# Optimization experiments

Hardware: AMD Instinct MI355X
Metric: run time of the kernel (lower is better)

## Reference

```python
import jax, jax.numpy as jnp
import numpy as np

N_NODES = 50000
N_EDGES = 800000
IN_DIM = 128
HID = 32
HEADS = 4
OUT_DIM = 64
NEG_SLOPE = 0.2


def _glorot(key, shape):
    fan = shape[0] + shape[-1] if len(shape) > 1 else shape[-1]
    lim = jnp.sqrt(6.0 / fan)
    return jax.random.uniform(key, shape, jnp.float32, -lim, lim)


def setup_inputs() -> dict:
    key = jax.random.key(0)
    ks = jax.random.split(key, 10)
    x = jax.random.normal(ks[0], (N_NODES, IN_DIM), jnp.float32)
    edge_index = jax.random.randint(ks[1], (2, N_EDGES), 0, N_NODES, jnp.int32)
    # layer 1: in=IN_DIM, heads=HEADS, out=HID, concat
    W1 = _glorot(ks[2], (IN_DIM, HEADS * HID))
    a_src1 = _glorot(ks[3], (HEADS, HID))
    a_dst1 = _glorot(ks[4], (HEADS, HID))
    b1 = jnp.zeros((HEADS * HID,), jnp.float32)
    # layer 2: in=HEADS*HID, heads=1, out=OUT_DIM, mean
    W2 = _glorot(ks[5], (HEADS * HID, OUT_DIM))
    a_src2 = _glorot(ks[6], (1, OUT_DIM))
    a_dst2 = _glorot(ks[7], (1, OUT_DIM))
    b2 = jnp.zeros((OUT_DIM,), jnp.float32)
    return {"x": x, "edge_index": edge_index, "W1": W1, "a_src1": a_src1,
            "a_dst1": a_dst1, "b1": b1, "W2": W2, "a_src2": a_src2,
            "a_dst2": a_dst2, "b2": b2}


def gat_conv(x, src, dst, W, a_src, a_dst, bias, heads, out_ch, concat, num_nodes):
    # x: [N, in]; src/dst: [E] (self-loops already included)
    h = (x @ W).reshape(num_nodes, heads, out_ch)          # [N, H, F]
    alpha_s = jnp.einsum('nhf,hf->nh', h, a_src)           # [N, H]
    alpha_d = jnp.einsum('nhf,hf->nh', h, a_dst)
    e = alpha_s[src] + alpha_d[dst]                        # [E, H]
    e = jnp.where(e >= 0, e, NEG_SLOPE * e)                # leaky relu
    # segment softmax over destination neighborhoods
    e_max = jax.ops.segment_max(e, dst, num_segments=num_nodes)
    ex = jnp.exp(e - e_max[dst])
    denom = jax.ops.segment_sum(ex, dst, num_segments=num_nodes)
    alpha = ex / (denom[dst] + 1e-16)                      # [E, H]
    msg = h[src] * alpha[:, :, None]                       # [E, H, F]
    out = jax.ops.segment_sum(msg, dst, num_segments=num_nodes)  # [N, H, F]
    if concat:
        out = out.reshape(num_nodes, heads * out_ch)
    else:
        out = out.mean(axis=1)
    return out + bias


def reference(x, edge_index, W1, a_src1, a_dst1, b1, W2, a_src2, a_dst2, b2):
    n = x.shape[0]
    # PyG GATConv default add_self_loops=True
    loop = jnp.arange(n, dtype=edge_index.dtype)
    src = jnp.concatenate([edge_index[0], loop])
    dst = jnp.concatenate([edge_index[1], loop])
    h = gat_conv(x, src, dst, W1, a_src1, a_dst1, b1, HEADS, HID, True, n)
    h = jax.nn.relu(h)
    out = gat_conv(h, src, dst, W2, a_src2, a_dst2, b2, 1, OUT_DIM, False, n)
    return out
```

## Files before the change

kernel.cpp:

```cpp
#include <hip/hip_runtime.h>
#include <hip/hip_fp16.h>
#include <math.h>


#define NEG_SLOPE 0.2f
#define CAP 64

__device__ __forceinline__ float lrelu_exp(float e) {
    e = (e >= 0.f) ? e : NEG_SLOPE * e;
    return __expf(e);
}

__global__ __launch_bounds__(256) void build_kernel(
    const float* __restrict__ x, const float* __restrict__ W1,
    const float* __restrict__ a_src1, const float* __restrict__ a_dst1,
    __half* __restrict__ h1h, float* __restrict__ as1, float* __restrict__ ad1,
    const int* __restrict__ src, const int* __restrict__ dst,
    int* __restrict__ deg, unsigned short* __restrict__ col,
    int N, int E, int Gg) {
    __shared__ float Ws[32 * 128];
    __shared__ float xs[64 * 32];
    const int tid = threadIdx.x;

    if (blockIdx.x >= Gg) {
        const int base = (blockIdx.x - Gg) * 2048 + tid * 8;
        int s[8], d[8];
        if (base + 8 <= E) {
            int4 a0 = *(const int4*)&src[base];
            int4 a1 = *(const int4*)&src[base + 4];
            int4 c0 = *(const int4*)&dst[base];
            int4 c1 = *(const int4*)&dst[base + 4];
            s[0]=a0.x; s[1]=a0.y; s[2]=a0.z; s[3]=a0.w;
            s[4]=a1.x; s[5]=a1.y; s[6]=a1.z; s[7]=a1.w;
            d[0]=c0.x; d[1]=c0.y; d[2]=c0.z; d[3]=c0.w;
            d[4]=c1.x; d[5]=c1.y; d[6]=c1.z; d[7]=c1.w;
        } else {
#pragma unroll
            for (int u = 0; u < 8; ++u) {
                int i = base + u;
                if (i < E) { s[u] = src[i]; d[u] = dst[i]; }
                else       { s[u] = -1;     d[u] = -1; }
            }
        }
        int p[8];
#pragma unroll
        for (int u = 0; u < 8; ++u)
            if (d[u] >= 0) p[u] = atomicAdd(&deg[d[u]], 1);
#pragma unroll
        for (int u = 0; u < 8; ++u)
            if (d[u] >= 0 && p[u] < CAP)
                col[d[u] * CAP + p[u]] = (unsigned short)s[u];
        return;
    }

    const int tf = tid & 31;
    const int tn = tid >> 5;
    const int nb = blockIdx.x * 64;
    float acc[8][4];
#pragma unroll
    for (int i = 0; i < 8; ++i)
#pragma unroll
        for (int j = 0; j < 4; ++j) acc[i][j] = 0.f;

    for (int kc = 0; kc < 128; kc += 32) {
#pragma unroll
        for (int l = 0; l < 4; ++l) {
            int idx = tid + l * 256;
            int k = idx >> 5, f4 = idx & 31;
            *(float4*)&Ws[k * 128 + f4 * 4] =
                *(const float4*)&W1[(kc + k) * 128 + f4 * 4];
        }
#pragma unroll
        for (int l = 0; l < 2; ++l) {
            int idx = tid + l * 256;
            int n = idx >> 3, j = idx & 7;
            int gn = nb + n; if (gn >= N) gn = N - 1;
            *(float4*)&xs[n * 32 + j * 4] =
                *(const float4*)&x[gn * 128 + kc + j * 4];
        }
        __syncthreads();
#pragma unroll
        for (int k = 0; k < 32; ++k) {
            float4 w = *(const float4*)&Ws[k * 128 + tf * 4];
#pragma unroll
            for (int i = 0; i < 8; ++i) {
                float xv = xs[(tn * 8 + i) * 32 + k];
                acc[i][0] += xv * w.x; acc[i][1] += xv * w.y;
                acc[i][2] += xv * w.z; acc[i][3] += xv * w.w;
            }
        }
        __syncthreads();
    }
    float4 asv = *(const float4*)&a_src1[tf * 4];
    float4 adv = *(const float4*)&a_dst1[tf * 4];
    const int head = tf >> 3;
    const int lane8 = tf & 7;
#pragma unroll
    for (int i = 0; i < 8; ++i) {
        int n = nb + tn * 8 + i;
        if (n < N) {
            __half2 p0 = __floats2half2_rn(acc[i][0], acc[i][1]);
            __half2 p1 = __floats2half2_rn(acc[i][2], acc[i][3]);
            uint2 pk;
            pk.x = *(unsigned*)&p0;
            pk.y = *(unsigned*)&p1;
            *(uint2*)&h1h[(size_t)n * 128 + tf * 4] = pk;
        }
        float s = acc[i][0]*asv.x + acc[i][1]*asv.y + acc[i][2]*asv.z + acc[i][3]*asv.w;
        float d = acc[i][0]*adv.x + acc[i][1]*adv.y + acc[i][2]*adv.z + acc[i][3]*adv.w;
        s += __shfl_down(s, 4); d += __shfl_down(d, 4);
        s += __shfl_down(s, 2); d += __shfl_down(d, 2);
        s += __shfl_down(s, 1); d += __shfl_down(d, 1);
        if (lane8 == 0 && n < N) { as1[n * 4 + head] = s; ad1[n * 4 + head] = d; }
    }
}

__global__ __launch_bounds__(256, 4) void agg1mm_kernel(
    const __half2* __restrict__ h1h2, const float* __restrict__ as1,
    const float* __restrict__ ad1, const float* __restrict__ b1,
    const float* __restrict__ W2, const float* __restrict__ a_src2,
    const float* __restrict__ a_dst2, const int* __restrict__ deg,
    const unsigned short* __restrict__ col,
    __half* __restrict__ h2h, float* __restrict__ as2, float* __restrict__ ad2,
    int N) {
    __shared__ float wls[4][4][68];
    __shared__ int   cls[4][64];
    __shared__ float hrs[4][128];
    __shared__ float part[16][64];
    const int tid = threadIdx.x;
    const int w = tid >> 6;
    const int lane = tid & 63;
    const int d = blockIdx.x * 4 + w;

    if (d < N) {
        const int hsel = lane >> 4;
        const float4 ad4 = *(const float4*)&ad1[4 * d];
        const float4 asd = *(const float4*)&as1[4 * d];
        const float adh = (hsel == 0) ? ad4.x : (hsel == 1) ? ad4.y
                        : (hsel == 2) ? ad4.z : ad4.w;
        const float ash = (hsel == 0) ? asd.x : (hsel == 1) ? asd.y
                        : (hsel == 2) ? asd.z : asd.w;
        const int dg = min(deg[d], CAP);
        const int dgp = (dg + 31) & ~31;
        const int beg = d * CAP;

        if (lane < dgp) {
            if (lane < dg) {
                int s = (int)col[beg + lane];
                cls[w][lane] = s;
                float4 a4 = *(const float4*)&as1[4 * s];
                wls[w][0][lane] = lrelu_exp(a4.x + ad4.x);
                wls[w][1][lane] = lrelu_exp(a4.y + ad4.y);
                wls[w][2][lane] = lrelu_exp(a4.z + ad4.z);
                wls[w][3][lane] = lrelu_exp(a4.w + ad4.w);
            } else {
                cls[w][lane] = 0;
                wls[w][0][lane] = 0.f;
                wls[w][1][lane] = 0.f;
                wls[w][2][lane] = 0.f;
                wls[w][3][lane] = 0.f;
            }
        }

        float wself = lrelu_exp(ash + adh);
        float2 vself = __half22float2(h1h2[((unsigned)d << 6) | (unsigned)lane]);
        float den = wself, accx = wself * vself.x, accy = wself * vself.y;

        for (int jj = 0; jj < dgp; jj += 32) {
            int ss[32];
#pragma unroll
            for (int q = 0; q < 8; ++q)
                *(int4*)&ss[q * 4] = *(const int4*)&cls[w][jj + q * 4];
            __half2 v[32];
#pragma unroll
            for (int u = 0; u < 32; ++u)
                v[u] = h1h2[(((unsigned)ss[u]) << 6) | (unsigned)lane];
            float wt[32];
#pragma unroll
            for (int q = 0; q < 8; ++q)
                *(float4*)&wt[q * 4] = *(const float4*)&wls[w][hsel][jj + q * 4];
#pragma unroll
            for (int u = 0; u < 32; ++u) {
                float2 vf = __half22float2(v[u]);
                den += wt[u];
                accx = fmaf(wt[u], vf.x, accx);
                accy = fmaf(wt[u], vf.y, accy);
            }
        }
        const float inv = 1.f / (den + 1e-16f);
        float2 bv = *(const float2*)&b1[lane * 2];
        float2 o;
        o.x = fmaxf(fmaf(accx, inv, bv.x), 0.f);
        o.y = fmaxf(fmaf(accy, inv, bv.y), 0.f);
        *(float2*)&hrs[w][lane * 2] = o;
    } else {
        hrs[w][lane * 2] = 0.f;
        hrs[w][lane * 2 + 1] = 0.f;
    }
    __syncthreads();

    float p0 = 0.f, p1 = 0.f, p2 = 0.f, p3 = 0.f;
#pragma unroll
    for (int kk = 0; kk < 32; kk += 4) {
        const int k = w * 32 + kk;
        float4 h0 = *(const float4*)&hrs[0][k];
        float4 h1 = *(const float4*)&hrs[1][k];
        float4 h2 = *(const float4*)&hrs[2][k];
        float4 h3 = *(const float4*)&hrs[3][k];
        float wv0 = W2[(k + 0) * 64 + lane];
        float wv1 = W2[(k + 1) * 64 + lane];
        float wv2 = W2[(k + 2) * 64 + lane];
        float wv3 = W2[(k + 3) * 64 + lane];
        p0 += h0.x * wv0 + h0.y * wv1 + h0.z * wv2 + h0.w * wv3;
        p1 += h1.x * wv0 + h1.y * wv1 + h1.z * wv2 + h1.w * wv3;
        p2 += h2.x * wv0 + h2.y * wv1 + h2.z * wv2 + h2.w * wv3;
        p3 += h3.x * wv0 + h3.y * wv1 + h3.z * wv2 + h3.w * wv3;
    }
    part[w * 4 + 0][lane] = p0;
    part[w * 4 + 1][lane] = p1;
    part[w * 4 + 2][lane] = p2;
    part[w * 4 + 3][lane] = p3;
    __syncthreads();

    if (d < N) {
        float h2f = part[0 * 4 + w][lane] + part[1 * 4 + w][lane] +
                    part[2 * 4 + w][lane] + part[3 * 4 + w][lane];
        h2h[((unsigned)d << 6) | (unsigned)lane] = __float2half(h2f);
        float s = h2f * a_src2[lane];
        float dv = h2f * a_dst2[lane];
        s += __shfl_down(s, 32); dv += __shfl_down(dv, 32);
        s += __shfl_down(s, 16); dv += __shfl_down(dv, 16);
        s += __shfl_down(s, 8);  dv += __shfl_down(dv, 8);
        s += __shfl_down(s, 4);  dv += __shfl_down(dv, 4);
        s += __shfl_down(s, 2);  dv += __shfl_down(dv, 2);
        s += __shfl_down(s, 1);  dv += __shfl_down(dv, 1);
        if (lane == 0) { as2[d] = s; ad2[d] = dv; }
    }
}

__global__ __launch_bounds__(256, 4) void agg2_kernel(
    const __half* __restrict__ h2h, const float* __restrict__ as2,
    const float* __restrict__ ad2, const float* __restrict__ b2,
    const int* __restrict__ deg, const unsigned short* __restrict__ col,
    float* __restrict__ out, int N) {
    __shared__ int   cls[4][64];
    __shared__ float wl[4][64];
    const int lane = threadIdx.x & 63;
    const int w = threadIdx.x >> 6;
    const int d = blockIdx.x * 4 + w;
    if (d >= N) return;
    const int dg = min(deg[d], CAP);
    const int dgp = (dg + 31) & ~31;
    const int beg = d * CAP;
    const float adv = ad2[d];

    float wself = lrelu_exp(as2[d] + adv);
    float den = wself;
    float acc = wself * __half2float(h2h[((unsigned)d << 6) | (unsigned)lane]);

    if (lane < dgp) {
        if (lane < dg) {
            int s = (int)col[beg + lane];
            cls[w][lane] = s;
            wl[w][lane] = lrelu_exp(as2[s] + adv);
        } else {
            cls[w][lane] = 0;
            wl[w][lane] = 0.f;
        }
    }

    for (int jj = 0; jj < dgp; jj += 32) {
        int ss[32];
#pragma unroll
        for (int q = 0; q < 8; ++q)
            *(int4*)&ss[q * 4] = *(const int4*)&cls[w][jj + q * 4];
        __half v[32];
#pragma unroll
        for (int u = 0; u < 32; ++u)
            v[u] = h2h[(((unsigned)ss[u]) << 6) | (unsigned)lane];
        float wt[32];
#pragma unroll
        for (int q = 0; q < 8; ++q)
            *(float4*)&wt[q * 4] = *(const float4*)&wl[w][jj + q * 4];
#pragma unroll
        for (int u = 0; u < 32; ++u) {
            den += wt[u];
            acc = fmaf(wt[u], __half2float(v[u]), acc);
        }
    }
    out[(size_t)d * 64 + lane] = acc / (den + 1e-16f) + b2[lane];
}

extern "C" void kernel_launch(void* const* d_in, const int* in_sizes, int n_in,
                              void* d_out, int out_size, void* d_ws, size_t ws_size,
                              hipStream_t stream) {
    const float* x      = (const float*)d_in[0];
    const int*   eidx   = (const int*)d_in[1];
    const float* W1     = (const float*)d_in[2];
    const float* a_src1 = (const float*)d_in[3];
    const float* a_dst1 = (const float*)d_in[4];
    const float* b1     = (const float*)d_in[5];
    const float* W2     = (const float*)d_in[6];
    const float* a_src2 = (const float*)d_in[7];
    const float* a_dst2 = (const float*)d_in[8];
    const float* b2     = (const float*)d_in[9];
    float* out = (float*)d_out;

    const int N = in_sizes[0] / 128;
    const int E = in_sizes[1] / 2;

    const int* src = eidx;
    const int* dst = eidx + E;

    float* ws_f = (float*)d_ws;
    float* as1 = ws_f;
    float* ad1 = as1 + (size_t)N * 4;
    float* as2 = ad1 + (size_t)N * 4;
    float* ad2 = as2 + (size_t)N;
    __half* h1h = (__half*)(ad2 + (size_t)N);
    __half* h2h = h1h + (size_t)N * 128;
    int* deg = (int*)(h2h + (size_t)N * 64);
    unsigned short* col = (unsigned short*)(deg + N);

    const int Gg = (N + 63) / 64;
    const int Gs = (E + 2047) / 2048;

    hipMemsetAsync(deg, 0, (size_t)N * sizeof(int), stream);

    build_kernel<<<Gg + Gs, 256, 0, stream>>>(x, W1, a_src1, a_dst1,
                                              h1h, as1, ad1,
                                              src, dst, deg, col, N, E, Gg);

    agg1mm_kernel<<<(N + 3) / 4, 256, 0, stream>>>(
        (const __half2*)h1h, as1, ad1, b1, W2, a_src2, a_dst2,
        deg, col, h2h, as2, ad2, N);

    agg2_kernel<<<(N + 3) / 4, 256, 0, stream>>>(h2h, as2, ad2, b2,
                                                 deg, col, out, N);
}
```

Measured before the change: 207.4 us.

## Partition edge scatter by destination range and use fp16 dot2 for layer-2 matmul

```diff
diff --git a/kernel.cpp b/kernel.cpp
--- a/kernel.cpp
+++ b/kernel.cpp
@@ -9,6 +9,16 @@
 __device__ __forceinline__ float lrelu_exp(float e) {
     e = (e >= 0.f) ? e : NEG_SLOPE * e;
     return __expf(e);
+}
+
+typedef _Float16 half2v __attribute__((ext_vector_type(2)));
+__device__ __forceinline__ float fdot2(__half2 a, __half2 b, float c) {
+#if __has_builtin(__builtin_amdgcn_fdot2)
+    return __builtin_amdgcn_fdot2(*(half2v*)&a, *(half2v*)&b, c, false);
+#else
+    float2 af = __half22float2(a), bf = __half22float2(b);
+    return fmaf(af.x, bf.x, fmaf(af.y, bf.y, c));
+#endif
 }
 
 __global__ __launch_bounds__(256) void build_kernel(
@@ -17,13 +27,29 @@
     __half* __restrict__ h1h, float* __restrict__ as1, float* __restrict__ ad1,
     const int* __restrict__ src, const int* __restrict__ dst,
     int* __restrict__ deg, unsigned short* __restrict__ col,
-    int N, int E, int Gg) {
+    const float* __restrict__ W2, __half2* __restrict__ W2p,
+    int N, int E, int Gg, int Gs8) {
     __shared__ float Ws[32 * 128];
     __shared__ float xs[64 * 32];
     const int tid = threadIdx.x;
 
+    if (blockIdx.x >= Gg + Gs8) {
+#pragma unroll
+        for (int it = 0; it < 16; ++it) {
+            int idx = it * 256 + tid;
+            int kp = idx >> 6, n = idx & 63;
+            W2p[idx] = __floats2half2_rn(W2[(2 * kp) * 64 + n],
+                                         (W2[(2 * kp + 1) * 64 + n]));
+        }
+        return;
+    }
+
     if (blockIdx.x >= Gg) {
-        const int base = (blockIdx.x - Gg) * 2048 + tid * 8;
+        const int part = blockIdx.x & 7;
+        const int stripe = (blockIdx.x - Gg) >> 3;
+        const int psz = (N + 7) / 8;
+        const int dlo = part * psz;
+        const int base = stripe * 2048 + tid * 8;
         int s[8], d[8];
         if (base + 8 <= E) {
             int4 a0 = *(const int4*)&src[base];
@@ -39,17 +65,16 @@
             for (int u = 0; u < 8; ++u) {
                 int i = base + u;
                 if (i < E) { s[u] = src[i]; d[u] = dst[i]; }
-                else       { s[u] = -1;     d[u] = -1; }
-            }
-        }
-        int p[8];
-#pragma unroll
-        for (int u = 0; u < 8; ++u)
-            if (d[u] >= 0) p[u] = atomicAdd(&deg[d[u]], 1);
-#pragma unroll
-        for (int u = 0; u < 8; ++u)
-            if (d[u] >= 0 && p[u] < CAP)
-                col[d[u] * CAP + p[u]] = (unsigned short)s[u];
+                else       { s[u] = -1;     d[u] = -(1 << 30); }
+            }
+        }
+#pragma unroll
+        for (int u = 0; u < 8; ++u) {
+            if ((unsigned)(d[u] - dlo) < (unsigned)psz) {
+                int p = atomicAdd(&deg[d[u]], 1);
+                if (p < CAP) col[d[u] * CAP + p] = (unsigned short)s[u];
+            }
+        }
         return;
     }
 
@@ -118,15 +143,15 @@
 __global__ __launch_bounds__(256, 4) void agg1mm_kernel(
     const __half2* __restrict__ h1h2, const float* __restrict__ as1,
     const float* __restrict__ ad1, const float* __restrict__ b1,
-    const float* __restrict__ W2, const float* __restrict__ a_src2,
+    const __half2* __restrict__ W2p, const float* __restrict__ a_src2,
     const float* __restrict__ a_dst2, const int* __restrict__ deg,
     const unsigned short* __restrict__ col,
     __half* __restrict__ h2h, float* __restrict__ as2, float* __restrict__ ad2,
     int N) {
-    __shared__ float wls[4][4][68];
-    __shared__ int   cls[4][64];
-    __shared__ float hrs[4][128];
-    __shared__ float part[16][64];
+    __shared__ float   wls[4][4][68];
+    __shared__ int     cls[4][64];
+    __shared__ __half2 hrs2[4][64];
+    __shared__ float   part[16][64];
     const int tid = threadIdx.x;
     const int w = tid >> 6;
     const int lane = tid & 63;
@@ -189,32 +214,23 @@
         }
         const float inv = 1.f / (den + 1e-16f);
         float2 bv = *(const float2*)&b1[lane * 2];
-        float2 o;
-        o.x = fmaxf(fmaf(accx, inv, bv.x), 0.f);
-        o.y = fmaxf(fmaf(accy, inv, bv.y), 0.f);
-        *(float2*)&hrs[w][lane * 2] = o;
+        float ox = fmaxf(fmaf(accx, inv, bv.x), 0.f);
+        float oy = fmaxf(fmaf(accy, inv, bv.y), 0.f);
+        hrs2[w][lane] = __floats2half2_rn(ox, oy);
     } else {
-        hrs[w][lane * 2] = 0.f;
-        hrs[w][lane * 2 + 1] = 0.f;
+        hrs2[w][lane] = __floats2half2_rn(0.f, 0.f);
     }
     __syncthreads();
 
     float p0 = 0.f, p1 = 0.f, p2 = 0.f, p3 = 0.f;
 #pragma unroll
-    for (int kk = 0; kk < 32; kk += 4) {
-        const int k = w * 32 + kk;
-        float4 h0 = *(const float4*)&hrs[0][k];
-        float4 h1 = *(const float4*)&hrs[1][k];
-        float4 h2 = *(const float4*)&hrs[2][k];
-        float4 h3 = *(const float4*)&hrs[3][k];
-        float wv0 = W2[(k + 0) * 64 + lane];
-        float wv1 = W2[(k + 1) * 64 + lane];
-        float wv2 = W2[(k + 2) * 64 + lane];
-        float wv3 = W2[(k + 3) * 64 + lane];
-        p0 += h0.x * wv0 + h0.y * wv1 + h0.z * wv2 + h0.w * wv3;
-        p1 += h1.x * wv0 + h1.y * wv1 + h1.z * wv2 + h1.w * wv3;
-        p2 += h2.x * wv0 + h2.y * wv1 + h2.z * wv2 + h2.w * wv3;
-        p3 += h3.x * wv0 + h3.y * wv1 + h3.z * wv2 + h3.w * wv3;
+    for (int i = 0; i < 16; ++i) {
+        const int kp = w * 16 + i;
+        __half2 wv = W2p[kp * 64 + lane];
+        p0 = fdot2(hrs2[0][kp], wv, p0);
+        p1 = fdot2(hrs2[1][kp], wv, p1);
+        p2 = fdot2(hrs2[2][kp], wv, p2);
+        p3 = fdot2(hrs2[3][kp], wv, p3);
     }
     part[w * 4 + 0][lane] = p0;
     part[w * 4 + 1][lane] = p1;
@@ -321,18 +337,20 @@
     __half* h2h = h1h + (size_t)N * 128;
     int* deg = (int*)(h2h + (size_t)N * 64);
     unsigned short* col = (unsigned short*)(deg + N);
+    __half2* W2p = (__half2*)(col + (size_t)N * CAP);
 
     const int Gg = (N + 63) / 64;
-    const int Gs = (E + 2047) / 2048;
+    const int Gs8 = ((E + 2047) / 2048) * 8;
 
     hipMemsetAsync(deg, 0, (size_t)N * sizeof(int), stream);
 
-    build_kernel<<<Gg + Gs, 256, 0, stream>>>(x, W1, a_src1, a_dst1,
-                                              h1h, as1, ad1,
-                                              src, dst, deg, col, N, E, Gg);
+    build_kernel<<<Gg + Gs8 + 1, 256, 0, stream>>>(x, W1, a_src1, a_dst1,
+                                                   h1h, as1, ad1,
+                                                   src, dst, deg, col,
+                                                   W2, W2p, N, E, Gg, Gs8);
 
     agg1mm_kernel<<<(N + 3) / 4, 256, 0, stream>>>(
-        (const __half2*)h1h, as1, ad1, b1, W2, a_src2, a_dst2,
+        (const __half2*)h1h, as1, ad1, b1, W2p, a_src2, a_dst2,
         deg, col, h2h, as2, ad2, N);
 
     agg2_kernel<<<(N + 3) / 4, 256, 0, stream>>>(h2h, as2, ad2, b2,
```

Result: faster. 200.6 us (-3.3%).
